# Optimization experiments

Hardware: AMD Instinct MI355X
Metric: run time of the kernel (lower is better)

The kernel has to match this reference:

```python
import jax, jax.numpy as jnp
import numpy as np


def setup_inputs() -> dict:
    key = jax.random.key(0)
    ks = jax.random.split(key, 8)
    B, W, H, C = 4, 64, 64, 256
    C2 = C // 2
    s = 0.05
    x = jax.random.normal(ks[0], (B, W, H, C), dtype=jnp.float32)
    Wq = jax.random.normal(ks[1], (C, C2), dtype=jnp.float32) * s
    bq = jax.random.normal(ks[2], (C2,), dtype=jnp.float32) * s
    Wk = jax.random.normal(ks[3], (C, C2), dtype=jnp.float32) * s
    bk = jax.random.normal(ks[4], (C2,), dtype=jnp.float32) * s
    Wv = jax.random.normal(ks[5], (C, C), dtype=jnp.float32) * s
    bv = jax.random.normal(ks[6], (C,), dtype=jnp.float32) * s
    # gamma is initialized to 0 in the original; use a nonzero value so the
    # attention branch actually contributes (math is identical).
    gamma = jnp.array([0.5], dtype=jnp.float32)
    return {"x": x, "Wq": Wq, "bq": bq, "Wk": Wk, "bk": bk, "Wv": Wv, "bv": bv, "gamma": gamma}


def reference(x, Wq, bq, Wk, bk, Wv, bv, gamma):
    B, W, H, C = x.shape
    N = W * H
    # 1x1 convs == per-pixel linear projections
    q = jnp.einsum('bwhc,cd->bwhd', x, Wq) + bq   # [B,W,H,C/2]
    k = jnp.einsum('bwhc,cd->bwhd', x, Wk) + bk   # [B,W,H,C/2]
    v = jnp.einsum('bwhc,cd->bwhd', x, Wv) + bv   # [B,W,H,C]
    # Faithful to original: raw row-major reshape (B,W,H,Cq) -> (B,Cq,N)
    # (this mixes spatial and channel axes, exactly as the TF code does)
    pq = q.reshape(B, -1, N)                      # [B,C/2,N]
    pk = k.reshape(B, -1, N)                      # [B,C/2,N]
    pv = v.reshape(B, -1, N)                      # [B,C,N]
    energy = jnp.einsum('bcn,bcm->bnm', pq, pk)   # [B,N,N] (pq transposed)
    attention = jax.nn.softmax(energy, axis=-1)   # [B,N,N]
    out = jnp.einsum('bcm,bnm->bcn', pv, attention)  # pv @ attention^T
    out = out.reshape(B, W, H, C)
    return gamma * out + x
```

## Files before the change

### kernel.cpp

```cpp
#include <hip/hip_runtime.h>
#include <hip/hip_bf16.h>
#include <stdint.h>


typedef __attribute__((ext_vector_type(8)))  short short8;
typedef __attribute__((ext_vector_type(4)))  float f32x4;
typedef __attribute__((ext_vector_type(16))) float f32x16;
typedef __attribute__((ext_vector_type(4)))  unsigned short u16x4;

#define MFMA16 __builtin_amdgcn_mfma_f32_16x16x32_bf16
#define MFMA32 __builtin_amdgcn_mfma_f32_32x32x16_bf16

__device__ __forceinline__ unsigned short f2bf(float f) {
    union { float f; uint32_t u; } v; v.f = f;
    return (unsigned short)((v.u + 0x8000u) >> 16);
}
__device__ __forceinline__ float bf2f(unsigned short h) {
    union { uint32_t u; float f; } v; v.u = ((uint32_t)h) << 16;
    return v.f;
}
__device__ __forceinline__ uint32_t pkbf(float a, float b) {
    union { __hip_bfloat162 h; uint32_t u; } v;
    v.h = __float22bfloat162_rn(float2{a, b});
    return v.u;
}

__global__ void prep_w(const float* __restrict__ Wq, const float* __restrict__ bq,
                       const float* __restrict__ Wk, const float* __restrict__ bk,
                       const float* __restrict__ Wv, const float* __restrict__ bv,
                       unsigned short* __restrict__ Wt, float* __restrict__ bias) {
    int g = blockIdx.x * 256 + threadIdx.x;
    int c = g & 255, d = g >> 8;
    float val;
    if (d < 128)      val = Wq[c * 128 + d];
    else if (d < 256) val = Wk[c * 128 + (d - 128)];
    else              val = Wv[c * 256 + (d - 256)];
    Wt[d * 256 + c] = f2bf(val);
    if (g < 512) {
        float bb;
        if (g < 128)      bb = bq[g];
        else if (g < 256) bb = bk[g - 128];
        else              bb = bv[g - 256];
        bias[g] = bb;
    }
}

__global__ __launch_bounds__(256) void proj(
        const float* __restrict__ x, const unsigned short* __restrict__ Wt,
        const float* __restrict__ bias,
        unsigned short* __restrict__ Qrm, unsigned short* __restrict__ Kp,
        unsigned short* __restrict__ Vp) {
    __shared__ unsigned short T[128 * 136];
    int bid = blockIdx.x;
    int tid = threadIdx.x;
    int wave = tid >> 6, lane = tid & 63;
    int l16 = lane & 15, quad = lane >> 4;

    int kind, b, a, vh = 0;
    if (bid < 256) { kind = bid >> 7; int s = bid & 127; b = s >> 5; a = s & 31; }
    else           { kind = 2; int s = bid - 256; vh = s >> 7; b = (s >> 5) & 3; a = s & 31; }

    short8 af[2][8];
    #pragma unroll
    for (int g = 0; g < 2; ++g) {
        int p_local = wave * 32 + g * 16 + l16;
        int pix = (kind == 2) ? (b * 4096 + a * 128 + p_local)
                              : (b * 4096 + a + 32 * p_local);
        const float* xr = x + (size_t)pix * 256;
        #pragma unroll
        for (int kk = 0; kk < 8; ++kk) {
            f32x4 u0 = *(const f32x4*)(xr + kk * 32 + quad * 8);
            f32x4 u1 = *(const f32x4*)(xr + kk * 32 + quad * 8 + 4);
            union { short8 s; uint32_t u[4]; } h;
            h.u[0] = pkbf(u0[0], u0[1]); h.u[1] = pkbf(u0[2], u0[3]);
            h.u[2] = pkbf(u1[0], u1[1]); h.u[3] = pkbf(u1[2], u1[3]);
            af[g][kk] = h.s;
        }
    }

    if (kind < 2) {
        int dbase = kind * 128;
        #pragma unroll 1
        for (int dt = 0; dt < 8; ++dt) {
            int d = dbase + dt * 16 + l16;
            float bval = bias[d];
            f32x4 acc0 = {0.f,0.f,0.f,0.f}, acc1 = {0.f,0.f,0.f,0.f};
            #pragma unroll
            for (int kk = 0; kk < 8; ++kk) {
                short8 wrow = *(const short8*)(Wt + d * 256 + kk * 32 + quad * 8);
                acc0 = MFMA16(af[0][kk], wrow, acc0, 0, 0, 0);
                acc1 = MFMA16(af[1][kk], wrow, acc1, 0, 0, 0);
            }
            #pragma unroll
            for (int g = 0; g < 2; ++g) {
                f32x4 acc = g ? acc1 : acc0;
                union { u16x4 v; uint32_t u[2]; } pk;
                pk.u[0] = pkbf(acc[0] + bval, acc[1] + bval);
                pk.u[1] = pkbf(acc[2] + bval, acc[3] + bval);
                *(u16x4*)(T + (dt * 16 + l16) * 136 + wave * 32 + g * 16 + quad * 4) = pk.v;
            }
        }
        __syncthreads();
        if (kind == 0) {
            unsigned short* ob = Qrm + (b << 19) + a * 128 * 128;
            #pragma unroll
            for (int it = 0; it < 8; ++it) {
                int ci = it * 256 + tid;
                int row = ci >> 4, cj = ci & 15;
                *(short8*)(ob + row * 128 + cj * 8) = *(const short8*)(T + row * 136 + cj * 8);
            }
        } else {
            unsigned short* kb = Kp + (b << 19);
            #pragma unroll
            for (int it = 0; it < 8; ++it) {
                int ci = it * 256 + tid;
                int row = ci >> 4, cj = ci & 15;
                *(short8*)(kb + (cj >> 1) * 65536 + (a * 128 + row) * 16 + (cj & 1) * 8)
                    = *(const short8*)(T + row * 136 + cj * 8);
            }
        }
    } else {
        #pragma unroll 1
        for (int dt = 0; dt < 8; ++dt) {
            int d = 256 + vh * 128 + dt * 16 + l16;
            f32x4 acc0 = {0.f,0.f,0.f,0.f}, acc1 = {0.f,0.f,0.f,0.f};
            #pragma unroll
            for (int kk = 0; kk < 8; ++kk) {
                short8 wrow = *(const short8*)(Wt + d * 256 + kk * 32 + quad * 8);
                acc0 = MFMA16(wrow, af[0][kk], acc0, 0, 0, 0);
                acc1 = MFMA16(wrow, af[1][kk], acc1, 0, 0, 0);
            }
            int dvl = dt * 16 + quad * 4;
            f32x4 bv4 = *(const f32x4*)(bias + 256 + vh * 128 + dvl);
            #pragma unroll
            for (int g = 0; g < 2; ++g) {
                f32x4 acc = g ? acc1 : acc0;
                union { u16x4 v; uint32_t u[2]; } pk;
                pk.u[0] = pkbf(acc[0] + bv4[0], acc[1] + bv4[1]);
                pk.u[1] = pkbf(acc[2] + bv4[2], acc[3] + bv4[3]);
                int p_local = wave * 32 + g * 16 + l16;
                *(u16x4*)(T + p_local * 136 + dvl) = pk.v;
            }
        }
        __syncthreads();
        unsigned short* vb = Vp + (b << 20);
        #pragma unroll
        for (int it = 0; it < 8; ++it) {
            int cid = it * 256 + tid;
            int c_local = cid >> 8, w = cid & 255;
            int p_local = c_local * 16 + (w >> 4);
            int chunk = (w >> 4) * 16 + vh * 8 + ((w & 15) >> 1);
            *(short8*)(vb + chunk * 4096 + (a * 8 + c_local) * 16 + (w & 1) * 8)
                = *(const short8*)(T + p_local * 136 + (w & 15) * 8);
        }
    }
}

__global__ __launch_bounds__(256, 2) void attn(
        const unsigned short* __restrict__ Qrm, const unsigned short* __restrict__ Kp,
        const unsigned short* __restrict__ Vp, unsigned short* __restrict__ Opart,
        float* __restrict__ Lpart) {
    __shared__ unsigned short Ps[2 * 64 * 72];

    int bid = blockIdx.x;
    int comb = bid & 7, qt = bid >> 3;
    int b = comb >> 1, ks = comb & 1;
    int tid = threadIdx.x, wave = tid >> 6, lane = tid & 63;
    int l32 = lane & 31, half = lane >> 5;
    int mt = wave & 1, nt = wave >> 1;

    const unsigned short* Qb = Qrm + (b << 19);
    const unsigned short* Kb = Kp + (b << 19);
    const unsigned short* Vb = Vp + (b << 20);

    int q0 = qt * 64;

    short8 qf[8];
    {
        const unsigned short* qrow = Qb + (q0 + nt * 32 + l32) * 128 + half * 8;
        #pragma unroll
        for (int kk = 0; kk < 8; ++kk) qf[kk] = *(const short8*)(qrow + kk * 16);
    }

    f32x16 O[2][2];
    #pragma unroll
    for (int i = 0; i < 2; ++i)
        #pragma unroll
        for (int j = 0; j < 2; ++j)
            #pragma unroll
            for (int r = 0; r < 16; ++r) O[i][j][r] = 0.f;
    float l_run = 0.f;

    const int m_base = ks * 2048;
    const int chunk_base = ks * 128;
    const int kbase = (m_base + mt * 32 + l32) * 16 + half * 8;

    short8 kf[8];
    #pragma unroll
    for (int kk = 0; kk < 8; ++kk)
        kf[kk] = *(const short8*)(Kb + kk * 65536 + kbase);
    short8 vfrag[2][4];
    #pragma unroll
    for (int c2 = 0; c2 < 2; ++c2)
        #pragma unroll
        for (int k2 = 0; k2 < 4; ++k2)
            vfrag[c2][k2] = *(const short8*)(Vb + (chunk_base + k2) * 4096
                              + ((wave * 2 + c2) * 32 + l32) * 16 + half * 8);
    {
        f32x16 S;
        #pragma unroll
        for (int r = 0; r < 16; ++r) S[r] = 0.f;
        #pragma unroll
        for (int kk = 0; kk < 8; ++kk) S = MFMA32(kf[kk], qf[kk], S, 0, 0, 0);
        #pragma unroll
        for (int g = 0; g < 4; ++g) {
            float p0 = __expf(S[g * 4 + 0]), p1 = __expf(S[g * 4 + 1]);
            float p2 = __expf(S[g * 4 + 2]), p3 = __expf(S[g * 4 + 3]);
            l_run += (p0 + p1) + (p2 + p3);
            union { u16x4 v; uint32_t u[2]; } pk;
            pk.u[0] = pkbf(p0, p1); pk.u[1] = pkbf(p2, p3);
            *(u16x4*)(Ps + (nt * 32 + l32) * 72 + mt * 32 + g * 8 + half * 4) = pk.v;
        }
        #pragma unroll
        for (int kk = 0; kk < 8; ++kk)
            kf[kk] = *(const short8*)(Kb + kk * 65536 + 64 * 16 + kbase);
    }

    #pragma unroll 1
    for (int kt = 0; kt < 32; ++kt) {
        __syncthreads();

        if (kt < 31) {
            f32x16 S;
            #pragma unroll
            for (int r = 0; r < 16; ++r) S[r] = 0.f;
            #pragma unroll
            for (int kk = 0; kk < 8; ++kk) S = MFMA32(kf[kk], qf[kk], S, 0, 0, 0);
            if (kt < 30) {
                int kr = (kt + 2) * 64 * 16 + kbase;
                #pragma unroll
                for (int kk = 0; kk < 8; ++kk)
                    kf[kk] = *(const short8*)(Kb + kk * 65536 + kr);
            }
            unsigned short* Pn = Ps + ((kt + 1) & 1) * (64 * 72);
            #pragma unroll
            for (int g = 0; g < 4; ++g) {
                float p0 = __expf(S[g * 4 + 0]), p1 = __expf(S[g * 4 + 1]);
                float p2 = __expf(S[g * 4 + 2]), p3 = __expf(S[g * 4 + 3]);
                l_run += (p0 + p1) + (p2 + p3);
                union { u16x4 v; uint32_t u[2]; } pk;
                pk.u[0] = pkbf(p0, p1); pk.u[1] = pkbf(p2, p3);
                *(u16x4*)(Pn + (nt * 32 + l32) * 72 + mt * 32 + g * 8 + half * 4) = pk.v;
            }
        }

        unsigned short* Pb = Ps + (kt & 1) * (64 * 72);
        #pragma unroll
        for (int k2 = 0; k2 < 4; ++k2) {
            short8 pa0 = *(const short8*)(Pb + (l32) * 72 + k2 * 16 + half * 8);
            short8 pa1 = *(const short8*)(Pb + (32 + l32) * 72 + k2 * 16 + half * 8);
            O[0][0] = MFMA32(pa0, vfrag[0][k2], O[0][0], 0, 0, 0);
            O[0][1] = MFMA32(pa0, vfrag[1][k2], O[0][1], 0, 0, 0);
            O[1][0] = MFMA32(pa1, vfrag[0][k2], O[1][0], 0, 0, 0);
            O[1][1] = MFMA32(pa1, vfrag[1][k2], O[1][1], 0, 0, 0);
        }

        if (kt < 31) {
            int ch1 = chunk_base + (kt + 1) * 4;
            #pragma unroll
            for (int c2 = 0; c2 < 2; ++c2)
                #pragma unroll
                for (int k2 = 0; k2 < 4; ++k2)
                    vfrag[c2][k2] = *(const short8*)(Vb + (ch1 + k2) * 4096
                                      + ((wave * 2 + c2) * 32 + l32) * 16 + half * 8);
        }
    }

    l_run += __shfl_xor(l_run, 32);
    unsigned short* Op = Opart + ((size_t)(ks * 4 + b) << 20);
    #pragma unroll
    for (int q2 = 0; q2 < 2; ++q2)
        #pragma unroll
        for (int c2 = 0; c2 < 2; ++c2) {
            int c = (wave * 2 + c2) * 32 + l32;
            #pragma unroll
            for (int r = 0; r < 16; ++r) {
                int n = q0 + q2 * 32 + (r & 3) + 8 * (r >> 2) + 4 * half;
                Op[(size_t)n * 256 + c] = f2bf(O[q2][c2][r]);
            }
        }
    if (half == 0) {
        int n = q0 + nt * 32 + l32;
        Lpart[((ks * 2 + mt) * 4 + b) * 4096 + n] = l_run;
    }
}

__global__ __launch_bounds__(256) void merge_out(
        const unsigned short* __restrict__ Opart, const float* __restrict__ Lpart,
        const float* __restrict__ x, const float* __restrict__ gamma,
        float* __restrict__ out) {
    __shared__ float tile[64 * 257];
    __shared__ float wsm[64];
    int b  = blockIdx.x >> 6;
    int n0 = (blockIdx.x & 63) << 6;
    int tid = threadIdx.x;
    float g = gamma[0];
    if (tid < 64) {
        int n = n0 + tid;
        float L = 0.f;
        #pragma unroll
        for (int s = 0; s < 4; ++s) L += Lpart[(s * 4 + b) * 4096 + n];
        wsm[tid] = g / L;
    }
    __syncthreads();
    int nl1 = tid >> 5, cb1 = (tid & 31) * 8;
    const unsigned short* Op0 = Opart + ((size_t)b << 20);
    const unsigned short* Op1 = Opart + ((size_t)(4 + b) << 20);
    #pragma unroll
    for (int i = 0; i < 8; ++i) {
        int nl = i * 8 + nl1;
        size_t off = (size_t)(n0 + nl) * 256 + cb1;
        short8 o0 = *(const short8*)(Op0 + off);
        short8 o1 = *(const short8*)(Op1 + off);
        float w = wsm[nl];
        float* tr = tile + nl * 257 + cb1;
        #pragma unroll
        for (int e = 0; e < 8; ++e)
            tr[e] = (bf2f((unsigned short)o0[e]) + bf2f((unsigned short)o1[e])) * w;
    }
    __syncthreads();
    int cg = tid >> 4, nq = (tid & 15) * 4;
    #pragma unroll
    for (int it = 0; it < 16; ++it) {
        int c = it * 16 + cg;
        size_t idx = ((size_t)b << 20) + (size_t)c * 4096 + n0 + nq;
        f32x4 xv = *(const f32x4*)(x + idx);
        f32x4 ov;
        #pragma unroll
        for (int e = 0; e < 4; ++e) ov[e] = tile[(nq + e) * 257 + c] + xv[e];
        *(f32x4*)(out + idx) = ov;
    }
}

extern "C" void kernel_launch(void* const* d_in, const int* in_sizes, int n_in,
                              void* d_out, int out_size, void* d_ws, size_t ws_size,
                              hipStream_t stream) {
    const float* x     = (const float*)d_in[0];
    const float* Wq    = (const float*)d_in[1];
    const float* bq    = (const float*)d_in[2];
    const float* Wk    = (const float*)d_in[3];
    const float* bk    = (const float*)d_in[4];
    const float* Wv    = (const float*)d_in[5];
    const float* bv    = (const float*)d_in[6];
    const float* gamma = (const float*)d_in[7];
    float* out = (float*)d_out;

    if (ws_size < 34080768u) return;

    char* ws = (char*)d_ws;
    unsigned short* Wt    = (unsigned short*)(ws);
    float*          bias  = (float*)        (ws +   262144);
    unsigned short* Qrm   = (unsigned short*)(ws +   264192);
    unsigned short* Kp    = (unsigned short*)(ws +  4458496);
    unsigned short* Vp    = (unsigned short*)(ws +  8652800);
    unsigned short* Opart = (unsigned short*)(ws + 17041408);
    float*          Lpart = (float*)        (ws + 33818624);

    prep_w   <<<512, 256, 0, stream>>>(Wq, bq, Wk, bk, Wv, bv, Wt, bias);
    proj     <<<512, 256, 0, stream>>>(x, Wt, bias, Qrm, Kp, Vp);
    attn     <<<512, 256, 0, stream>>>(Qrm, Kp, Vp, Opart, Lpart);
    merge_out<<<256, 256, 0, stream>>>(Opart, Lpart, x, gamma, out);
}
```

Baseline: 172.5 us.

## Fuse merge into attention via last-block atomic counter and double-buffer V fragments

Removes the separate merge_out kernel. Each attention block bumps an atomic counter per (query tile, batch), and whichever of the two key-split blocks finishes second does the normalization, transpose and residual add, reusing the P shared buffer as the transpose tile. V fragments are now double-buffered in registers and prefetched at the start of each iteration rather than after the PV MFMAs. This saves one launch and overlaps the merge with other blocks' attention work, at the cost of more registers, shared memory and a threadfence/atomic handshake.

```diff
diff --git a/kernel.cpp b/kernel.cpp
--- a/kernel.cpp
+++ b/kernel.cpp
@@ -28,7 +28,8 @@
 __global__ void prep_w(const float* __restrict__ Wq, const float* __restrict__ bq,
                        const float* __restrict__ Wk, const float* __restrict__ bk,
                        const float* __restrict__ Wv, const float* __restrict__ bv,
-                       unsigned short* __restrict__ Wt, float* __restrict__ bias) {
+                       unsigned short* __restrict__ Wt, float* __restrict__ bias,
+                       int* __restrict__ cnt) {
     int g = blockIdx.x * 256 + threadIdx.x;
     int c = g & 255, d = g >> 8;
     float val;
@@ -43,6 +44,7 @@
         else              bb = bv[g - 256];
         bias[g] = bb;
     }
+    if (g < 256) cnt[g] = 0;
 }
 
 __global__ __launch_bounds__(256) void proj(
@@ -159,8 +161,14 @@
 __global__ __launch_bounds__(256, 2) void attn(
         const unsigned short* __restrict__ Qrm, const unsigned short* __restrict__ Kp,
         const unsigned short* __restrict__ Vp, unsigned short* __restrict__ Opart,
-        float* __restrict__ Lpart) {
-    __shared__ unsigned short Ps[2 * 64 * 72];
+        float* __restrict__ Lpart, const float* __restrict__ x,
+        const float* __restrict__ gamma, float* __restrict__ out,
+        int* __restrict__ cnt) {
+    __shared__ __align__(16) char smem[32896];
+    __shared__ float wsm[64];
+    __shared__ int who;
+    unsigned short* Ps = (unsigned short*)smem;
+    float* tile = (float*)smem;
 
     int bid = blockIdx.x;
     int comb = bid & 7, qt = bid >> 3;
@@ -194,18 +202,19 @@
     const int m_base = ks * 2048;
     const int chunk_base = ks * 128;
     const int kbase = (m_base + mt * 32 + l32) * 16 + half * 8;
+    const int vbase = (wave * 64 + l32) * 16 + half * 8;
 
     short8 kf[8];
     #pragma unroll
     for (int kk = 0; kk < 8; ++kk)
         kf[kk] = *(const short8*)(Kb + kk * 65536 + kbase);
-    short8 vfrag[2][4];
+    short8 vfrag[2][2][4];
     #pragma unroll
     for (int c2 = 0; c2 < 2; ++c2)
         #pragma unroll
         for (int k2 = 0; k2 < 4; ++k2)
-            vfrag[c2][k2] = *(const short8*)(Vb + (chunk_base + k2) * 4096
-                              + ((wave * 2 + c2) * 32 + l32) * 16 + half * 8);
+            vfrag[0][c2][k2] = *(const short8*)(Vb + (chunk_base + k2) * 4096
+                                 + vbase + c2 * 512);
     {
         f32x16 S;
         #pragma unroll
@@ -231,6 +240,16 @@
         __syncthreads();
 
         if (kt < 31) {
+            int ch1 = chunk_base + (kt + 1) * 4;
+            #pragma unroll
+            for (int c2 = 0; c2 < 2; ++c2)
+                #pragma unroll
+                for (int k2 = 0; k2 < 4; ++k2)
+                    vfrag[(kt + 1) & 1][c2][k2] =
+                        *(const short8*)(Vb + (ch1 + k2) * 4096 + vbase + c2 * 512);
+        }
+
+        if (kt < 31) {
             f32x16 S;
             #pragma unroll
             for (int r = 0; r < 16; ++r) S[r] = 0.f;
@@ -259,20 +278,10 @@
         for (int k2 = 0; k2 < 4; ++k2) {
             short8 pa0 = *(const short8*)(Pb + (l32) * 72 + k2 * 16 + half * 8);
             short8 pa1 = *(const short8*)(Pb + (32 + l32) * 72 + k2 * 16 + half * 8);
-            O[0][0] = MFMA32(pa0, vfrag[0][k2], O[0][0], 0, 0, 0);
-            O[0][1] = MFMA32(pa0, vfrag[1][k2], O[0][1], 0, 0, 0);
-            O[1][0] = MFMA32(pa1, vfrag[0][k2], O[1][0], 0, 0, 0);
-            O[1][1] = MFMA32(pa1, vfrag[1][k2], O[1][1], 0, 0, 0);
-        }
-
-        if (kt < 31) {
-            int ch1 = chunk_base + (kt + 1) * 4;
-            #pragma unroll
-            for (int c2 = 0; c2 < 2; ++c2)
-                #pragma unroll
-                for (int k2 = 0; k2 < 4; ++k2)
-                    vfrag[c2][k2] = *(const short8*)(Vb + (ch1 + k2) * 4096
-                                      + ((wave * 2 + c2) * 32 + l32) * 16 + half * 8);
+            O[0][0] = MFMA32(pa0, vfrag[kt & 1][0][k2], O[0][0], 0, 0, 0);
+            O[0][1] = MFMA32(pa0, vfrag[kt & 1][1][k2], O[0][1], 0, 0, 0);
+            O[1][0] = MFMA32(pa1, vfrag[kt & 1][0][k2], O[1][0], 0, 0, 0);
+            O[1][1] = MFMA32(pa1, vfrag[kt & 1][1][k2], O[1][1], 0, 0, 0);
         }
     }
 
@@ -293,52 +302,55 @@
         int n = q0 + nt * 32 + l32;
         Lpart[((ks * 2 + mt) * 4 + b) * 4096 + n] = l_run;
     }
-}
-
-__global__ __launch_bounds__(256) void merge_out(
-        const unsigned short* __restrict__ Opart, const float* __restrict__ Lpart,
-        const float* __restrict__ x, const float* __restrict__ gamma,
-        float* __restrict__ out) {
-    __shared__ float tile[64 * 257];
-    __shared__ float wsm[64];
-    int b  = blockIdx.x >> 6;
-    int n0 = (blockIdx.x & 63) << 6;
-    int tid = threadIdx.x;
+
+    __threadfence();
+    __syncthreads();
+    if (tid == 0) who = (atomicAdd(&cnt[qt * 4 + b], 1) == 1);
+    __syncthreads();
+    if (!who) return;
+    __threadfence();
+
     float g = gamma[0];
     if (tid < 64) {
-        int n = n0 + tid;
+        int n = q0 + tid;
         float L = 0.f;
         #pragma unroll
         for (int s = 0; s < 4; ++s) L += Lpart[(s * 4 + b) * 4096 + n];
         wsm[tid] = g / L;
     }
     __syncthreads();
-    int nl1 = tid >> 5, cb1 = (tid & 31) * 8;
+
     const unsigned short* Op0 = Opart + ((size_t)b << 20);
     const unsigned short* Op1 = Opart + ((size_t)(4 + b) << 20);
-    #pragma unroll
-    for (int i = 0; i < 8; ++i) {
-        int nl = i * 8 + nl1;
-        size_t off = (size_t)(n0 + nl) * 256 + cb1;
-        short8 o0 = *(const short8*)(Op0 + off);
-        short8 o1 = *(const short8*)(Op1 + off);
-        float w = wsm[nl];
-        float* tr = tile + nl * 257 + cb1;
-        #pragma unroll
-        for (int e = 0; e < 8; ++e)
-            tr[e] = (bf2f((unsigned short)o0[e]) + bf2f((unsigned short)o1[e])) * w;
-    }
-    __syncthreads();
-    int cg = tid >> 4, nq = (tid & 15) * 4;
-    #pragma unroll
-    for (int it = 0; it < 16; ++it) {
-        int c = it * 16 + cg;
-        size_t idx = ((size_t)b << 20) + (size_t)c * 4096 + n0 + nq;
-        f32x4 xv = *(const f32x4*)(x + idx);
-        f32x4 ov;
-        #pragma unroll
-        for (int e = 0; e < 4; ++e) ov[e] = tile[(nq + e) * 257 + c] + xv[e];
-        *(f32x4*)(out + idx) = ov;
+    int nl1 = tid >> 5, cb1 = (tid & 31) * 8;
+    int cg = tid >> 3, nq = (tid & 7) * 4;
+    #pragma unroll 1
+    for (int ch = 0; ch < 2; ++ch) {
+        int nb = q0 + ch * 32;
+        #pragma unroll
+        for (int i = 0; i < 4; ++i) {
+            int nl = i * 8 + nl1;
+            size_t off = (size_t)(nb + nl) * 256 + cb1;
+            short8 o0 = *(const short8*)(Op0 + off);
+            short8 o1 = *(const short8*)(Op1 + off);
+            float w = wsm[ch * 32 + nl];
+            float* tr = tile + nl * 257 + cb1;
+            #pragma unroll
+            for (int e = 0; e < 8; ++e)
+                tr[e] = (bf2f((unsigned short)o0[e]) + bf2f((unsigned short)o1[e])) * w;
+        }
+        __syncthreads();
+        #pragma unroll
+        for (int it = 0; it < 8; ++it) {
+            int c = it * 32 + cg;
+            size_t idx = ((size_t)b << 20) + (size_t)c * 4096 + nb + nq;
+            f32x4 xv = *(const f32x4*)(x + idx);
+            f32x4 ov;
+            #pragma unroll
+            for (int e = 0; e < 4; ++e) ov[e] = tile[(nq + e) * 257 + c] + xv[e];
+            *(f32x4*)(out + idx) = ov;
+        }
+        __syncthreads();
     }
 }
 
@@ -355,7 +367,7 @@
     const float* gamma = (const float*)d_in[7];
     float* out = (float*)d_out;
 
-    if (ws_size < 34080768u) return;
+    if (ws_size < 34081792u) return;
 
     char* ws = (char*)d_ws;
     unsigned short* Wt    = (unsigned short*)(ws);
@@ -365,9 +377,9 @@
     unsigned short* Vp    = (unsigned short*)(ws +  8652800);
     unsigned short* Opart = (unsigned short*)(ws + 17041408);
     float*          Lpart = (float*)        (ws + 33818624);
-
-    prep_w   <<<512, 256, 0, stream>>>(Wq, bq, Wk, bk, Wv, bv, Wt, bias);
-    proj     <<<512, 256, 0, stream>>>(x, Wt, bias, Qrm, Kp, Vp);
-    attn     <<<512, 256, 0, stream>>>(Qrm, Kp, Vp, Opart, Lpart);
-    merge_out<<<256, 256, 0, stream>>>(Opart, Lpart, x, gamma, out);
-}
+    int*            cnt   = (int*)          (ws + 34080768);
+
+    prep_w<<<512, 256, 0, stream>>>(Wq, bq, Wk, bk, Wv, bv, Wt, bias, cnt);
+    proj  <<<512, 256, 0, stream>>>(x, Wt, bias, Qrm, Kp, Vp);
+    attn  <<<512, 256, 0, stream>>>(Qrm, Kp, Vp, Opart, Lpart, x, gamma, out, cnt);
+}
```

New measurement: 394.3 us. +128.5%, slower.
